# Kernel tuning notes

Measured on AMD Instinct MI355X. Metric: run time of the kernel, lower is better.

Reference implementation:

```python
import jax, jax.numpy as jnp
import numpy as np

N_NODES = 50000
N_EDGES = 1600000
IN_DIM = 64
HID = 64
EPS = 1e-5


def setup_inputs() -> dict:
    key = jax.random.key(0)
    ks = jax.random.split(key, 8)
    x = jax.random.normal(ks[0], (N_NODES, IN_DIM), dtype=jnp.float32)
    edge_index = jax.random.randint(ks[1], (2, N_EDGES), 0, N_NODES, dtype=jnp.int64)
    s1 = 1.0 / np.sqrt(IN_DIM)
    s2 = 1.0 / np.sqrt(HID)
    return {
        "x": x,
        "W1": jax.random.normal(ks[2], (IN_DIM, HID), jnp.float32) * s1,
        "b1": jnp.zeros((HID,), jnp.float32),
        "g1": jnp.ones((HID,), jnp.float32),
        "bt1": jnp.zeros((HID,), jnp.float32),
        "W2": jax.random.normal(ks[3], (HID, HID), jnp.float32) * s2,
        "b2": jnp.zeros((HID,), jnp.float32),
        "g2": jnp.ones((HID,), jnp.float32),
        "bt2": jnp.zeros((HID,), jnp.float32),
        "W3": jax.random.normal(ks[4], (HID, 1), jnp.float32) * s2,
        "b3": jnp.zeros((1,), jnp.float32),
        "edge_index": edge_index,
    }


def _gcn_conv(x, W, b, src, dst, norm, n):
    # GCNConv: D^{-1/2}(A+I)D^{-1/2} X W + b (self-loops already in src/dst)
    h = x @ W                                  # [N, out]
    msg = h[src] * norm[:, None]               # gather + scale, [E+N, out]
    out = jax.ops.segment_sum(msg, dst, num_segments=n)  # scatter-add
    return out + b


def _bn(x, gamma, beta):
    # BatchNorm1d training-mode stats over nodes (biased variance, as torch)
    mu = x.mean(axis=0)
    var = x.var(axis=0)
    return (x - mu) * jax.lax.rsqrt(var + EPS) * gamma + beta


def reference(x, W1, b1, g1, bt1, W2, b2, g2, bt2, W3, b3, edge_index):
    n = x.shape[0]
    loop = jnp.arange(n, dtype=edge_index.dtype)
    src = jnp.concatenate([edge_index[0], loop])
    dst = jnp.concatenate([edge_index[1], loop])
    deg = jax.ops.segment_sum(jnp.ones(src.shape[0], x.dtype), dst, num_segments=n)
    dinv = jnp.where(deg > 0, jax.lax.rsqrt(deg), 0.0)
    norm = dinv[src] * dinv[dst]

    h = jax.nn.relu(_bn(_gcn_conv(x, W1, b1, src, dst, norm, n), g1, bt1))
    h = jax.nn.relu(_bn(_gcn_conv(h, W2, b2, src, dst, norm, n), g2, bt2))
    out = _gcn_conv(h, W3, b3, src, dst, norm, n)
    return out.reshape(-1)
```

## Files before the change

### kernel.cpp

```cpp
#include <hip/hip_runtime.h>
#include <hip/hip_bf16.h>


__device__ __forceinline__ unsigned f2bf(float f) {
    unsigned u = __float_as_uint(f);
    return (u + 0x7FFFu + ((u >> 16) & 1u)) >> 16;
}
__device__ __forceinline__ float bflo(unsigned w) { return __uint_as_float(w << 16); }
__device__ __forceinline__ float bfhi(unsigned w) { return __uint_as_float(w & 0xFFFF0000u); }

__global__ void deg_count(const int* __restrict__ dst, int* __restrict__ degi, int E) {
    int tid = blockIdx.x * blockDim.x + threadIdx.x;
    int stride = gridDim.x * blockDim.x;
    for (int e = tid; e < E; e += stride) atomicAdd(&degi[dst[e]], 1);
}

__global__ void scan_part(const int* __restrict__ degi, int* __restrict__ part, int n) {
    __shared__ int ls[256];
    int i = blockIdx.x * 256 + threadIdx.x;
    ls[threadIdx.x] = (i < n) ? degi[i] : 0;
    __syncthreads();
    for (int o = 128; o > 0; o >>= 1) {
        if (threadIdx.x < o) ls[threadIdx.x] += ls[threadIdx.x + o];
        __syncthreads();
    }
    if (threadIdx.x == 0) part[blockIdx.x] = ls[0];
}

__global__ void scan_root(int* __restrict__ part, int nblk) {
    __shared__ int ls[256];
    int t = threadIdx.x;
    int v = (t < nblk) ? part[t] : 0;
    ls[t] = v;
    __syncthreads();
    for (int o = 1; o < 256; o <<= 1) {
        int u = (t >= o) ? ls[t - o] : 0;
        __syncthreads();
        ls[t] += u;
        __syncthreads();
    }
    if (t < nblk) part[t] = ls[t] - v;
}

__global__ void scan_write(const int* __restrict__ degi, const int* __restrict__ part,
                           int* __restrict__ off, int* __restrict__ cur,
                           float* __restrict__ dinv, int n) {
    __shared__ int ls[256];
    int t = threadIdx.x, i = blockIdx.x * 256 + t;
    int d = (i < n) ? degi[i] : 0;
    ls[t] = d;
    __syncthreads();
    for (int o = 1; o < 256; o <<= 1) {
        int u = (t >= o) ? ls[t - o] : 0;
        __syncthreads();
        ls[t] += u;
        __syncthreads();
    }
    if (i < n) {
        int o0 = part[blockIdx.x] + ls[t] - d;
        off[i] = o0;
        cur[i] = o0;
        dinv[i] = rsqrtf((float)d + 1.0f);
        if (i == n - 1) off[n] = o0 + d;
    }
}

__global__ void csr_fill_x(const int* __restrict__ src, const int* __restrict__ dst,
                           int* __restrict__ cur, int* __restrict__ csr, int E, int n) {
    int w = blockIdx.x & 7;
    int lo = (int)(((long long)n * w) >> 3);
    int hi = (int)(((long long)n * (w + 1)) >> 3);
    int tid = (blockIdx.x >> 3) * blockDim.x + threadIdx.x;
    int stride = (gridDim.x >> 3) * blockDim.x;
    for (int e = tid; e < E; e += stride) {
        int d = dst[e];
        if (d >= lo && d < hi) {
            int p = atomicAdd(&cur[d], 1);
            csr[p] = src[e];
        }
    }
}

__global__ void prescale(const float* __restrict__ x, const float* __restrict__ dinv,
                         unsigned* __restrict__ T, int n) {
    int tid = blockIdx.x * blockDim.x + threadIdx.x;
    int stride = gridDim.x * blockDim.x;
    int total = n * 32;
    const float2* x2 = (const float2*)x;
    for (int i = tid; i < total; i += stride) {
        float2 v = x2[i];
        float dv = dinv[i >> 5];
        T[i] = f2bf(v.x * dv) | (f2bf(v.y * dv) << 16);
    }
}

__global__ void bnrelu_scale(const float* __restrict__ Y, const double* __restrict__ stats,
                             const float* __restrict__ g, const float* __restrict__ bt,
                             const float* __restrict__ dinv, unsigned* __restrict__ T, int n) {
    int jj = threadIdx.x & 31;
    int f0 = jj * 2, f1 = jj * 2 + 1;
    double m0 = stats[f0] / n, m1 = stats[f1] / n;
    double v0 = stats[64 + f0] / n - m0 * m0, v1 = stats[64 + f1] / n - m1 * m1;
    float sc0 = (float)(1.0 / sqrt(v0 + 1e-5)) * g[f0];
    float sc1 = (float)(1.0 / sqrt(v1 + 1e-5)) * g[f1];
    float sh0 = bt[f0] - (float)m0 * sc0;
    float sh1 = bt[f1] - (float)m1 * sc1;
    const float2* Y2 = (const float2*)Y;
    int tid = blockIdx.x * blockDim.x + threadIdx.x;
    int stride = gridDim.x * blockDim.x;
    for (int i = tid; i < n * 32; i += stride) {
        float2 y = Y2[i];
        float dv = dinv[i >> 5];
        float a = fmaxf(y.x * sc0 + sh0, 0.f) * dv;
        float b = fmaxf(y.y * sc1 + sh1, 0.f) * dv;
        T[i] = f2bf(a) | (f2bf(b) << 16);
    }
}

__global__ __launch_bounds__(256) void agg_mm(
        const uint4* __restrict__ Tb, const int* __restrict__ csr,
        const int* __restrict__ off, const float* __restrict__ dinv,
        const float* __restrict__ W, const float* __restrict__ bias,
        double* __restrict__ stats_out, float* __restrict__ Y, int n) {
    __shared__ double ls[256], lq[256];

    int lane = threadIdx.x & 63;
    int slot = lane >> 3;
    int fl   = lane & 7;
    float bv = bias[lane];

    float w[64];
    #pragma unroll
    for (int k = 0; k < 64; ++k) w[k] = W[k * 64 + lane];

    int wave  = (blockIdx.x * blockDim.x + threadIdx.x) >> 6;
    int nwave = (gridDim.x * blockDim.x) >> 6;
    double s = 0.0, sq = 0.0;

    for (int i = wave; i < n; i += nwave) {
        int beg = off[i], end = off[i + 1];
        float dv = dinv[i];

        float4 al = {0,0,0,0}, ah = {0,0,0,0};
        if (slot == 0) {
            uint4 r = Tb[(size_t)i * 8 + fl];
            al.x = bflo(r.x); al.y = bfhi(r.x);
            al.z = bflo(r.y); al.w = bfhi(r.y);
            ah.x = bflo(r.z); ah.y = bfhi(r.z);
            ah.z = bflo(r.w); ah.w = bfhi(r.w);
        }

        #pragma unroll 2
        for (int c = beg + slot; c < end; c += 8) {
            int sr = csr[c];
            uint4 r = Tb[(size_t)sr * 8 + fl];
            al.x += bflo(r.x); al.y += bfhi(r.x);
            al.z += bflo(r.y); al.w += bfhi(r.y);
            ah.x += bflo(r.z); ah.y += bfhi(r.z);
            ah.z += bflo(r.w); ah.w += bfhi(r.w);
        }

        #pragma unroll
        for (int m = 8; m <= 32; m <<= 1) {
            al.x += __shfl_xor(al.x, m, 64); al.y += __shfl_xor(al.y, m, 64);
            al.z += __shfl_xor(al.z, m, 64); al.w += __shfl_xor(al.w, m, 64);
            ah.x += __shfl_xor(ah.x, m, 64); ah.y += __shfl_xor(ah.y, m, 64);
            ah.z += __shfl_xor(ah.z, m, 64); ah.w += __shfl_xor(ah.w, m, 64);
        }

        float acc = 0.f;
        #pragma unroll
        for (int k = 0; k < 64; ++k) {
            const int c = k & 7, sl = k >> 3;
            float comp = c == 0 ? al.x : c == 1 ? al.y : c == 2 ? al.z : c == 3 ? al.w
                       : c == 4 ? ah.x : c == 5 ? ah.y : c == 6 ? ah.z : ah.w;
            float sv = __uint_as_float(
                (unsigned)__builtin_amdgcn_readlane((int)__float_as_uint(comp), sl));
            acc = fmaf(sv, w[k], acc);
        }
        float yv = dv * acc + bv;
        Y[(size_t)i * 64 + lane] = yv;
        s += (double)yv; sq += (double)yv * (double)yv;
    }

    ls[threadIdx.x] = s; lq[threadIdx.x] = sq;
    __syncthreads();
    if (threadIdx.x < 64) {
        double ts = ls[threadIdx.x] + ls[threadIdx.x + 64] + ls[threadIdx.x + 128] + ls[threadIdx.x + 192];
        double tq = lq[threadIdx.x] + lq[threadIdx.x + 64] + lq[threadIdx.x + 128] + lq[threadIdx.x + 192];
        atomicAdd(&stats_out[threadIdx.x], ts);
        atomicAdd(&stats_out[64 + threadIdx.x], tq);
    }
}

__global__ void head_w3(const float* __restrict__ Y, const double* __restrict__ stats,
                        const float* __restrict__ g, const float* __restrict__ bt,
                        const float* __restrict__ W3, const float* __restrict__ dinv,
                        float* __restrict__ hs3, int n) {
    int lane = threadIdx.x & 63;
    double mean = stats[lane] / n;
    double var  = stats[64 + lane] / n - mean * mean;
    float scale = (float)(1.0 / sqrt(var + 1e-5)) * g[lane];
    float shift = bt[lane] - (float)mean * scale;
    float w = W3[lane];
    int wave  = (blockIdx.x * blockDim.x + threadIdx.x) >> 6;
    int nwave = (gridDim.x * blockDim.x) >> 6;
    for (int row = wave; row < n; row += nwave) {
        float v = fmaxf(Y[(size_t)row * 64 + lane] * scale + shift, 0.f) * w;
        #pragma unroll
        for (int o = 32; o > 0; o >>= 1) v += __shfl_down(v, o, 64);
        if (lane == 0) hs3[row] = v * dinv[row];
    }
}

__global__ void agg1(const float* __restrict__ hs3, const int* __restrict__ csr,
                     const int* __restrict__ off, const float* __restrict__ dinv,
                     const float* __restrict__ b3, float* __restrict__ out, int n) {
    float b = b3[0];
    int lane  = threadIdx.x & 63;
    int wave  = (blockIdx.x * blockDim.x + threadIdx.x) >> 6;
    int nwave = (gridDim.x * blockDim.x) >> 6;
    for (int i = wave; i < n; i += nwave) {
        int beg = off[i], end = off[i + 1];
        float acc = 0.f;
        for (int e = beg + lane; e < end; e += 64) acc += hs3[csr[e]];
        #pragma unroll
        for (int o = 32; o > 0; o >>= 1) acc += __shfl_down(acc, o, 64);
        if (lane == 0) out[i] = dinv[i] * (acc + hs3[i]) + b;
    }
}

extern "C" void kernel_launch(void* const* d_in, const int* in_sizes, int n_in,
                              void* d_out, int out_size, void* d_ws, size_t ws_size,
                              hipStream_t stream) {
    const float* x   = (const float*)d_in[0];
    const float* W1  = (const float*)d_in[1];
    const float* b1  = (const float*)d_in[2];
    const float* g1  = (const float*)d_in[3];
    const float* bt1 = (const float*)d_in[4];
    const float* W2  = (const float*)d_in[5];
    const float* b2  = (const float*)d_in[6];
    const float* g2  = (const float*)d_in[7];
    const float* bt2 = (const float*)d_in[8];
    const float* W3  = (const float*)d_in[9];
    const float* b3  = (const float*)d_in[10];
    const int*  edge = (const int*)d_in[11];

    int n = in_sizes[0] / 64;
    int E = in_sizes[11] / 2;
    const int* src = edge;
    const int* dst = edge + E;
    float* out = (float*)d_out;
    int nblk = (n + 255) / 256;

    char* p = (char*)d_ws;
    double* stats = (double*)p;            p += 256 * sizeof(double);
    float* dinv   = (float*)p;             p += ((n + 63) & ~63) * sizeof(float);
    int* degi     = (int*)p;               p += ((n + 63) & ~63) * sizeof(int);
    int* off      = (int*)p;               p += ((n + 64) & ~63) * sizeof(int);
    int* cur      = (int*)p;               p += ((n + 63) & ~63) * sizeof(int);
    int* part     = (int*)p;               p += 256 * sizeof(int);
    int* csr      = (int*)p;               p += (size_t)E * sizeof(int);
    unsigned* A   = (unsigned*)p;          p += (size_t)n * 32 * sizeof(unsigned);
    float* B      = (float*)p;             p += (size_t)n * 64 * sizeof(float);
    float* hs3    = (float*)p;

    hipMemsetAsync(degi, 0, n * sizeof(int), stream);
    hipMemsetAsync(stats, 0, 256 * sizeof(double), stream);

    deg_count<<<2048, 256, 0, stream>>>(dst, degi, E);
    scan_part<<<nblk, 256, 0, stream>>>(degi, part, n);
    scan_root<<<1, 256, 0, stream>>>(part, nblk);
    scan_write<<<nblk, 256, 0, stream>>>(degi, part, off, cur, dinv, n);
    csr_fill_x<<<2048, 256, 0, stream>>>(src, dst, cur, csr, E, n);

    prescale<<<1024, 256, 0, stream>>>(x, dinv, A, n);
    agg_mm<<<2048, 256, 0, stream>>>((const uint4*)A, csr, off, dinv, W1, b1,
                                     stats, B, n);
    bnrelu_scale<<<1024, 256, 0, stream>>>(B, stats, g1, bt1, dinv, A, n);
    agg_mm<<<2048, 256, 0, stream>>>((const uint4*)A, csr, off, dinv, W2, b2,
                                     stats + 128, B, n);
    head_w3<<<2048, 256, 0, stream>>>(B, stats + 128, g2, bt2, W3, dinv, hs3, n);
    agg1<<<2048, 256, 0, stream>>>(hs3, csr, off, dinv, b3, out, n);
}
```

Measured before the change: 339.6 us.

## Bin edges by destination window before degree count and CSR fill

Adds a binning pass that groups edges by destination-node window in shared memory and writes packed (local dst, src) words into per-window staging buffers aliased on an unused workspace array. Degree counting and CSR fill then run per window over the compact binned stream instead of rescanning the full edge list eight times with range filtering. This cuts edge-list traffic and localizes atomics, but packs src into 16 bits and assumes at most 8 windows, so it only holds for node counts below 65536.

```diff
diff --git a/kernel.cpp b/kernel.cpp
--- a/kernel.cpp
+++ b/kernel.cpp
@@ -9,10 +9,57 @@
 __device__ __forceinline__ float bflo(unsigned w) { return __uint_as_float(w << 16); }
 __device__ __forceinline__ float bfhi(unsigned w) { return __uint_as_float(w & 0xFFFF0000u); }
 
-__global__ void deg_count(const int* __restrict__ dst, int* __restrict__ degi, int E) {
-    int tid = blockIdx.x * blockDim.x + threadIdx.x;
-    int stride = gridDim.x * blockDim.x;
-    for (int e = tid; e < E; e += stride) atomicAdd(&degi[dst[e]], 1);
+#define WSH 13
+#define BCHUNK 2048
+
+__global__ __launch_bounds__(256) void binA(
+        const int* __restrict__ src, const int* __restrict__ dst,
+        int* __restrict__ gcur1, unsigned* __restrict__ st1,
+        int E, int cap1, int nwin) {
+    __shared__ unsigned buf[BCHUNK];
+    __shared__ int hist[8], base[8], pos[8];
+    int t = threadIdx.x;
+    int beg = blockIdx.x * BCHUNK;
+    int end = min(beg + BCHUNK, E);
+    if (beg >= end) return;
+    if (t < 8) hist[t] = 0;
+    __syncthreads();
+    for (int i = beg + t; i < end; i += 256)
+        atomicAdd(&hist[dst[i] >> WSH], 1);
+    __syncthreads();
+    if (t == 0) {
+        int acc = 0;
+        for (int w = 0; w < 8; ++w) { base[w] = acc; pos[w] = acc; acc += hist[w]; }
+    }
+    __syncthreads();
+    for (int i = beg + t; i < end; i += 256) {
+        int d = dst[i];
+        int p = atomicAdd(&pos[d >> WSH], 1);
+        buf[p] = ((unsigned)(d & ((1 << WSH) - 1)) << 16) | (unsigned)src[i];
+    }
+    __syncthreads();
+    int wave = t >> 6, lane = t & 63;
+    for (int w = wave; w < nwin; w += 4) {
+        int lo = base[w], cnt = pos[w] - lo;
+        if (cnt == 0) continue;
+        int g;
+        if (lane == 0) g = atomicAdd(&gcur1[w], cnt);
+        g = __shfl(g, 0, 64);
+        unsigned* outp = st1 + (size_t)w * cap1 + g;
+        for (int k = lane; k < cnt; k += 64) outp[k] = buf[lo + k];
+    }
+}
+
+__global__ void deg_s(const int* __restrict__ gcur1, const unsigned* __restrict__ st1,
+                      int* __restrict__ degi, int cap1, int nwin, int bpw) {
+    int w = blockIdx.x % nwin;
+    int sub = blockIdx.x / nwin;
+    int cnt = gcur1[w];
+    int lo = w << WSH;
+    const unsigned* in = st1 + (size_t)w * cap1;
+    int stride = bpw * blockDim.x;
+    for (int i = sub * blockDim.x + threadIdx.x; i < cnt; i += stride)
+        atomicAdd(&degi[lo + (in[i] >> 16)], 1);
 }
 
 __global__ void scan_part(const int* __restrict__ degi, int* __restrict__ part, int n) {
@@ -65,19 +112,20 @@
     }
 }
 
-__global__ void csr_fill_x(const int* __restrict__ src, const int* __restrict__ dst,
-                           int* __restrict__ cur, int* __restrict__ csr, int E, int n) {
-    int w = blockIdx.x & 7;
-    int lo = (int)(((long long)n * w) >> 3);
-    int hi = (int)(((long long)n * (w + 1)) >> 3);
-    int tid = (blockIdx.x >> 3) * blockDim.x + threadIdx.x;
-    int stride = (gridDim.x >> 3) * blockDim.x;
-    for (int e = tid; e < E; e += stride) {
-        int d = dst[e];
-        if (d >= lo && d < hi) {
-            int p = atomicAdd(&cur[d], 1);
-            csr[p] = src[e];
-        }
+__global__ void fillW(const int* __restrict__ gcur1, const unsigned* __restrict__ st1,
+                      int* __restrict__ cur, int* __restrict__ csr,
+                      int cap1, int nwin, int bpw) {
+    int w = blockIdx.x % nwin;
+    int sub = blockIdx.x / nwin;
+    int cnt = gcur1[w];
+    int lo = w << WSH;
+    const unsigned* in = st1 + (size_t)w * cap1;
+    int stride = bpw * blockDim.x;
+    for (int i = sub * blockDim.x + threadIdx.x; i < cnt; i += stride) {
+        unsigned e = in[i];
+        int d = lo + (int)(e >> 16);
+        int p = atomicAdd(&cur[d], 1);
+        csr[p] = (int)(e & 0xFFFFu);
     }
 }
 
@@ -252,6 +300,9 @@
     const int* dst = edge + E;
     float* out = (float*)d_out;
     int nblk = (n + 255) / 256;
+    int nwin = (n + (1 << WSH) - 1) >> WSH;
+    int cap1 = (E / nwin) * 5 / 4 + 1024;
+    int bpw  = 256;
 
     char* p = (char*)d_ws;
     double* stats = (double*)p;            p += 256 * sizeof(double);
@@ -260,19 +311,23 @@
     int* off      = (int*)p;               p += ((n + 64) & ~63) * sizeof(int);
     int* cur      = (int*)p;               p += ((n + 63) & ~63) * sizeof(int);
     int* part     = (int*)p;               p += 256 * sizeof(int);
+    int* gcur1    = (int*)p;               p += 64 * sizeof(int);
     int* csr      = (int*)p;               p += (size_t)E * sizeof(int);
     unsigned* A   = (unsigned*)p;          p += (size_t)n * 32 * sizeof(unsigned);
     float* B      = (float*)p;             p += (size_t)n * 64 * sizeof(float);
     float* hs3    = (float*)p;
+    unsigned* st1 = (unsigned*)B;
 
     hipMemsetAsync(degi, 0, n * sizeof(int), stream);
+    hipMemsetAsync(gcur1, 0, 64 * sizeof(int), stream);
     hipMemsetAsync(stats, 0, 256 * sizeof(double), stream);
 
-    deg_count<<<2048, 256, 0, stream>>>(dst, degi, E);
+    binA<<<(E + BCHUNK - 1) / BCHUNK, 256, 0, stream>>>(src, dst, gcur1, st1, E, cap1, nwin);
+    deg_s<<<nwin * bpw, 256, 0, stream>>>(gcur1, st1, degi, cap1, nwin, bpw);
     scan_part<<<nblk, 256, 0, stream>>>(degi, part, n);
     scan_root<<<1, 256, 0, stream>>>(part, nblk);
     scan_write<<<nblk, 256, 0, stream>>>(degi, part, off, cur, dinv, n);
-    csr_fill_x<<<2048, 256, 0, stream>>>(src, dst, cur, csr, E, n);
+    fillW<<<nwin * bpw, 256, 0, stream>>>(gcur1, st1, cur, csr, cap1, nwin, bpw);
 
     prescale<<<1024, 256, 0, stream>>>(x, dinv, A, n);
     agg_mm<<<2048, 256, 0, stream>>>((const uint4*)A, csr, off, dinv, W1, b1,
```

Result: slower. 465.5 us (+37.1%).
